# Kernel tuning notes

Measured on AMD Instinct MI355X. Metric: run time of the kernel, lower is better.

## Reference

```python
import jax, jax.numpy as jnp
import numpy as np

N_NODES = 100000
N_EDGES = 1600000
N_GRAPHS = 4096
IN_DIM = 14
HID = 128


def setup_inputs() -> dict:
    key = jax.random.key(0)
    ks = jax.random.split(key, 12)
    x = jax.random.normal(ks[0], (N_NODES, IN_DIM), dtype=jnp.float32)
    edge_index = jax.random.randint(ks[1], (2, N_EDGES), 0, N_NODES, dtype=jnp.int64)
    batch = jnp.sort(jax.random.randint(ks[2], (N_NODES,), 0, N_GRAPHS, dtype=jnp.int64))

    def lin(k, fan_in, fan_out):
        bound = 1.0 / np.sqrt(fan_in)
        kw, kb = jax.random.split(k)
        W = jax.random.uniform(kw, (fan_in, fan_out), minval=-bound, maxval=bound, dtype=jnp.float32)
        b = jax.random.uniform(kb, (fan_out,), minval=-bound, maxval=bound, dtype=jnp.float32)
        return W, b

    W1a, b1a = lin(ks[3], IN_DIM, HID)
    W1b, b1b = lin(ks[4], HID, HID)
    W2a, b2a = lin(ks[5], HID, HID)
    W2b, b2b = lin(ks[6], HID, HID)
    Wout, bout = lin(ks[7], HID, HID)
    return dict(x=x, edge_index=edge_index, batch=batch,
                W1a=W1a, b1a=b1a, W1b=W1b, b1b=b1b,
                W2a=W2a, b2a=b2a, W2b=W2b, b2b=b2b,
                Wout=Wout, bout=bout)


def _gin_conv(x, src, dst, Wa, ba, Wb, bb):
    # aggregate: sum of neighbor features x[src] scattered to dst; eps = 0
    agg = jax.ops.segment_sum(x[src], dst, num_segments=N_NODES)
    h = x + agg  # (1 + eps) * x + sum_j x_j, eps=0
    h = jax.nn.relu(h @ Wa + ba)
    return h @ Wb + bb


def reference(x, edge_index, batch, W1a, b1a, W1b, b1b, W2a, b2a, W2b, b2b, Wout, bout):
    src, dst = edge_index[0], edge_index[1]
    h = jax.nn.relu(_gin_conv(x, src, dst, W1a, b1a, W1b, b1b))
    h = jax.nn.relu(_gin_conv(h, src, dst, W2a, b2a, W2b, b2b))
    # global mean pool over graphs
    sums = jax.ops.segment_sum(h, batch, num_segments=N_GRAPHS)          # [G, HID]
    cnts = jax.ops.segment_sum(jnp.ones((h.shape[0],), h.dtype), batch, num_segments=N_GRAPHS)
    pooled = sums / jnp.maximum(cnts, 1.0)[:, None]
    # dropout is identity in eval mode
    return pooled @ Wout + bout
```

## Files before the change

kernel.cpp:

```cpp
#include <hip/hip_runtime.h>
#include <hip/hip_bf16.h>

#define NODES  100000
#define EDGES  1600000
#define GRAPHS 4096
#define HID    128
#define INDIM  14
#define NPART  8
#define PART_SZ ((NODES + NPART - 1) / NPART)
#define BPG    256
#define CSTRIDE 64
#define LDST   136
#define LDSTF  132

typedef float f32x4 __attribute__((ext_vector_type(4)));
typedef short bf16x8 __attribute__((ext_vector_type(8)));
typedef int   i32x4 __attribute__((ext_vector_type(4)));

__device__ __forceinline__ unsigned packbf(float a, float b) {
    __hip_bfloat162 t;
    t.x = __float2bfloat16(a);
    t.y = __float2bfloat16(b);
    return *(unsigned*)&t;
}
__device__ __forceinline__ void acc8(float* a, uint4 v) {
    a[0] += __uint_as_float(v.x << 16);
    a[1] += __uint_as_float(v.x & 0xffff0000u);
    a[2] += __uint_as_float(v.y << 16);
    a[3] += __uint_as_float(v.y & 0xffff0000u);
    a[4] += __uint_as_float(v.z << 16);
    a[5] += __uint_as_float(v.z & 0xffff0000u);
    a[6] += __uint_as_float(v.w << 16);
    a[7] += __uint_as_float(v.w & 0xffff0000u);
}


__global__ void k_zero2(int* __restrict__ cnt, float* __restrict__ pooled) {
    int i = blockIdx.x * 256 + threadIdx.x;
    if (i < NODES) cnt[i] = 0;
    if (i < GRAPHS * HID) pooled[i] = 0.f;
}


__global__ __launch_bounds__(256) void k_fill_fx(const i32x4* __restrict__ src4,
                                                 const i32x4* __restrict__ dst4,
                                                 int* __restrict__ cnt,
                                                 int* __restrict__ csr) {
    const int g = blockIdx.x & (NPART - 1);
    const int blk = blockIdx.x >> 3;
    const int lo = g * PART_SZ;
    const int n4 = EDGES / 4;
    for (int e4 = blk * 256 + threadIdx.x; e4 < n4; e4 += BPG * 256) {
        i32x4 d = __builtin_nontemporal_load(&dst4[e4]);
        i32x4 s = __builtin_nontemporal_load(&src4[e4]);
#pragma unroll
        for (int j = 0; j < 4; j++) {
            int dj = d[j];
            if ((unsigned)(dj - lo) < PART_SZ) {
                int pos = atomicAdd(&cnt[dj], 1);
                if (pos < CSTRIDE) csr[dj * CSTRIDE + pos] = s[j];
            }
        }
    }
}


__global__ void k_w_cvt4(const float* __restrict__ Wa, const float* __restrict__ Wb,
                         const float* __restrict__ Wc, const float* __restrict__ Wd,
                         __hip_bfloat16* __restrict__ Ta, __hip_bfloat16* __restrict__ Tb,
                         __hip_bfloat16* __restrict__ Tc, __hip_bfloat16* __restrict__ Td) {
    int which = blockIdx.x >> 6;
    int idx = (blockIdx.x & 63) * 256 + threadIdx.x;
    const float* W = which == 0 ? Wa : which == 1 ? Wb : which == 2 ? Wc : Wd;
    __hip_bfloat16* T = which == 0 ? Ta : which == 1 ? Tb : which == 2 ? Tc : Td;
    int n = idx & 127, k = idx >> 7;
    T[n * HID + k] = __float2bfloat16(W[k * HID + n]);
}


template <int RELU, int TO_LDS>
__device__ __forceinline__ void mfma_slice16(const __hip_bfloat16* lds_in,
                                             const __hip_bfloat16* __restrict__ Wt,
                                             const float* __restrict__ bias,
                                             __hip_bfloat16* lds_out,
                                             __hip_bfloat16* __restrict__ gout,
                                             int row0, int tid) {
    const int wave = tid >> 6;
    const int lane = tid & 63;
    const int rl = lane & 15;
    const int kb = lane >> 4;

    bf16x8 afrag[4];
#pragma unroll
    for (int kc = 0; kc < 4; kc++)
        afrag[kc] = *(const bf16x8*)(lds_in + rl * LDST + kc * 32 + kb * 8);

#pragma unroll
    for (int s = 0; s < 2; s++) {
        const int n = wave * 2 + s;
        f32x4 acc = (f32x4){0.f, 0.f, 0.f, 0.f};
        const __hip_bfloat16* Bp = Wt + (size_t)(n * 16 + rl) * HID + kb * 8;
#pragma unroll
        for (int kc = 0; kc < 4; kc++) {
            bf16x8 bfrag = *(const bf16x8*)(Bp + kc * 32);
            acc = __builtin_amdgcn_mfma_f32_16x16x32_bf16(afrag[kc], bfrag, acc, 0, 0, 0);
        }
        const int col = n * 16 + rl;
        const float bv = bias[col];
#pragma unroll
        for (int j = 0; j < 4; j++) {
            int rloc = kb * 4 + j;
            float v = acc[j] + bv;
            if (RELU) v = fmaxf(v, 0.f);
            if (TO_LDS)
                lds_out[rloc * LDST + col] = __float2bfloat16(v);
            else
                gout[(size_t)(row0 + rloc) * HID + col] = __float2bfloat16(v);
        }
    }
}


__global__ __launch_bounds__(256) void k_l1(const float* __restrict__ x,
                                            const int* __restrict__ cnt,
                                            const int* __restrict__ csr,
                                            const float* __restrict__ W1a,
                                            const float* __restrict__ b1a,
                                            const __hip_bfloat16* __restrict__ Wt1b,
                                            const float* __restrict__ b1b,
                                            __hip_bfloat16* __restrict__ h1) {
    __shared__ float p14[16][16];
    __shared__ __hip_bfloat16 t[16 * LDST];
    const int row0 = blockIdx.x * 16;
    const int tid = threadIdx.x;

    {
        int n = tid >> 4, d = tid & 15;
        int node = row0 + n;
        if (d < INDIM) {
            int len = cnt[node];
            if (len > CSTRIDE) len = CSTRIDE;
            const int* cp = csr + (size_t)node * CSTRIDE;
            float acc = x[node * INDIM + d];
            int e = 0;
            for (; e + 7 < len; e += 8) {
                int s0 = cp[e], s1 = cp[e + 1], s2 = cp[e + 2], s3 = cp[e + 3];
                int s4 = cp[e + 4], s5 = cp[e + 5], s6 = cp[e + 6], s7 = cp[e + 7];
                float v0 = x[s0 * INDIM + d], v1 = x[s1 * INDIM + d];
                float v2 = x[s2 * INDIM + d], v3 = x[s3 * INDIM + d];
                float v4 = x[s4 * INDIM + d], v5 = x[s5 * INDIM + d];
                float v6 = x[s6 * INDIM + d], v7 = x[s7 * INDIM + d];
                acc += ((v0 + v1) + (v2 + v3)) + ((v4 + v5) + (v6 + v7));
            }
            for (; e + 3 < len; e += 4) {
                int s0 = cp[e], s1 = cp[e + 1], s2 = cp[e + 2], s3 = cp[e + 3];
                acc += x[s0 * INDIM + d] + x[s1 * INDIM + d] +
                       x[s2 * INDIM + d] + x[s3 * INDIM + d];
            }
            for (; e < len; e++) acc += x[cp[e] * INDIM + d];
            p14[n][d] = acc;
        }
    }
    __syncthreads();

    for (int i = tid; i < 512; i += 256) {
        int r = i >> 5, c4 = (i & 31) << 2;
        float4 bv = *(const float4*)&b1a[c4];
        float ax = bv.x, ay = bv.y, az = bv.z, aw = bv.w;
#pragma unroll
        for (int k = 0; k < INDIM; k++) {
            float a = p14[r][k];
            float4 w = *(const float4*)&W1a[k * HID + c4];
            ax += a * w.x; ay += a * w.y; az += a * w.z; aw += a * w.w;
        }
        unsigned p0 = packbf(fmaxf(ax, 0.f), fmaxf(ay, 0.f));
        unsigned p1 = packbf(fmaxf(az, 0.f), fmaxf(aw, 0.f));
        *(uint2*)&t[r * LDST + c4] = make_uint2(p0, p1);
    }
    __syncthreads();

    mfma_slice16<1, 0>(t, Wt1b, b1b, nullptr, h1, row0, tid);
}


__global__ __launch_bounds__(256) void k_l2p(const uint4* __restrict__ H,
                                             const int* __restrict__ cnt,
                                             const int* __restrict__ csr,
                                             const int* __restrict__ batch,
                                             const __hip_bfloat16* __restrict__ Wt2a,
                                             const float* __restrict__ b2a,
                                             const __hip_bfloat16* __restrict__ Wt2b,
                                             const float* __restrict__ b2b,
                                             float* __restrict__ pooled) {
    __shared__ __hip_bfloat16 ta[16 * LDST];
    __shared__ __hip_bfloat16 tb[16 * LDST];
    __shared__ float t2f[16 * LDSTF];
    __shared__ int sb[16];
    const int row0 = blockIdx.x * 16;
    const int tid = threadIdx.x;

    if (tid < 16) sb[tid] = batch[row0 + tid];

    {
        int n = tid >> 4, q = tid & 15;
        int node = row0 + n;
        int len = cnt[node];
        if (len > CSTRIDE) len = CSTRIDE;
        const int* cp = csr + (size_t)node * CSTRIDE;
        float a[8];
        uint4 v = H[(size_t)node * 16 + q];
        a[0] = __uint_as_float(v.x << 16);
        a[1] = __uint_as_float(v.x & 0xffff0000u);
        a[2] = __uint_as_float(v.y << 16);
        a[3] = __uint_as_float(v.y & 0xffff0000u);
        a[4] = __uint_as_float(v.z << 16);
        a[5] = __uint_as_float(v.z & 0xffff0000u);
        a[6] = __uint_as_float(v.w << 16);
        a[7] = __uint_as_float(v.w & 0xffff0000u);
        int e = 0;
        for (; e + 7 < len; e += 8) {
            uint4 v0 = H[(size_t)cp[e + 0] * 16 + q];
            uint4 v1 = H[(size_t)cp[e + 1] * 16 + q];
            uint4 v2 = H[(size_t)cp[e + 2] * 16 + q];
            uint4 v3 = H[(size_t)cp[e + 3] * 16 + q];
            uint4 v4 = H[(size_t)cp[e + 4] * 16 + q];
            uint4 v5 = H[(size_t)cp[e + 5] * 16 + q];
            uint4 v6 = H[(size_t)cp[e + 6] * 16 + q];
            uint4 v7 = H[(size_t)cp[e + 7] * 16 + q];
            acc8(a, v0); acc8(a, v1); acc8(a, v2); acc8(a, v3);
            acc8(a, v4); acc8(a, v5); acc8(a, v6); acc8(a, v7);
        }
        for (; e + 3 < len; e += 4) {
            uint4 v0 = H[(size_t)cp[e + 0] * 16 + q];
            uint4 v1 = H[(size_t)cp[e + 1] * 16 + q];
            uint4 v2 = H[(size_t)cp[e + 2] * 16 + q];
            uint4 v3 = H[(size_t)cp[e + 3] * 16 + q];
            acc8(a, v0); acc8(a, v1); acc8(a, v2); acc8(a, v3);
        }
        for (; e < len; e++) {
            uint4 vv = H[(size_t)cp[e] * 16 + q];
            acc8(a, vv);
        }
        uint4 o;
        o.x = packbf(a[0], a[1]);
        o.y = packbf(a[2], a[3]);
        o.z = packbf(a[4], a[5]);
        o.w = packbf(a[6], a[7]);
        *(uint4*)&ta[n * LDST + q * 8] = o;
    }
    __syncthreads();

    mfma_slice16<1, 1>(ta, Wt2a, b2a, tb, nullptr, row0, tid);
    __syncthreads();

    {
        const int wave = tid >> 6;
        const int lane = tid & 63;
        const int rl = lane & 15;
        const int kb = lane >> 4;
        bf16x8 afrag[4];
#pragma unroll
        for (int kc = 0; kc < 4; kc++)
            afrag[kc] = *(const bf16x8*)(tb + rl * LDST + kc * 32 + kb * 8);
#pragma unroll
        for (int s = 0; s < 2; s++) {
            const int n = wave * 2 + s;
            f32x4 acc = (f32x4){0.f, 0.f, 0.f, 0.f};
            const __hip_bfloat16* Bp = Wt2b + (size_t)(n * 16 + rl) * HID + kb * 8;
#pragma unroll
            for (int kc = 0; kc < 4; kc++) {
                bf16x8 bfrag = *(const bf16x8*)(Bp + kc * 32);
                acc = __builtin_amdgcn_mfma_f32_16x16x32_bf16(afrag[kc], bfrag, acc, 0, 0, 0);
            }
            const int col = n * 16 + rl;
            const float bv = b2b[col];
#pragma unroll
            for (int j = 0; j < 4; j++)
                t2f[(kb * 4 + j) * LDSTF + col] = fmaxf(acc[j] + bv, 0.f);
        }
    }
    __syncthreads();

    {
        int c = tid & 127;
        int half = tid >> 7;
        int r0 = half * 8;
        float acc = t2f[r0 * LDSTF + c];
        int gprev = sb[r0];
        for (int r = r0 + 1; r < r0 + 8; r++) {
            int g = sb[r];
            float v = t2f[r * LDSTF + c];
            if (g != gprev) {
                atomicAdd(&pooled[(size_t)gprev * HID + c], acc);
                acc = 0.f;
                gprev = g;
            }
            acc += v;
        }
        atomicAdd(&pooled[(size_t)gprev * HID + c], acc);
    }
}


__device__ __forceinline__ int lower_bound_i(const int* __restrict__ a, int n, int key) {
    int lo = 0, hi = n;
    while (lo < hi) {
        int mid = (lo + hi) >> 1;
        if (a[mid] < key) lo = mid + 1; else hi = mid;
    }
    return lo;
}

__global__ __launch_bounds__(256) void k_head(const float* __restrict__ pooled,
                                              const int* __restrict__ batch,
                                              const __hip_bfloat16* __restrict__ Wt,
                                              const float* __restrict__ bias,
                                              float* __restrict__ out) {
    const int wave = threadIdx.x >> 6;
    const int lane = threadIdx.x & 63;
    const int row0 = blockIdx.x * 64 + wave * 16;
    const int rl = lane & 15;
    const int kb = lane >> 4;

    const int g = row0 + rl;
    int lo = lower_bound_i(batch, NODES, g);
    int hi = lower_bound_i(batch, NODES, g + 1);
    float inv = 1.0f / fmaxf((float)(hi - lo), 1.0f);

    bf16x8 afrag[4];
#pragma unroll
    for (int kc = 0; kc < 4; kc++) {
        const float* Ap = pooled + (size_t)g * HID + kc * 32 + kb * 8;
        unsigned u[4];
#pragma unroll
        for (int p = 0; p < 4; p++) u[p] = packbf(Ap[p * 2] * inv, Ap[p * 2 + 1] * inv);
        afrag[kc] = *(bf16x8*)u;
    }

#pragma unroll
    for (int n = 0; n < 8; n++) {
        f32x4 acc = (f32x4){0.f, 0.f, 0.f, 0.f};
        const __hip_bfloat16* Bp = Wt + (size_t)(n * 16 + rl) * HID + kb * 8;
#pragma unroll
        for (int kc = 0; kc < 4; kc++) {
            bf16x8 bfrag = *(const bf16x8*)(Bp + kc * 32);
            acc = __builtin_amdgcn_mfma_f32_16x16x32_bf16(afrag[kc], bfrag, acc, 0, 0, 0);
        }
        const int col = n * 16 + rl;
        const float bv = bias[col];
#pragma unroll
        for (int j = 0; j < 4; j++)
            out[(size_t)(row0 + kb * 4 + j) * HID + col] = acc[j] + bv;
    }
}


extern "C" void kernel_launch(void* const* d_in, const int* in_sizes, int n_in,
                              void* d_out, int out_size, void* d_ws, size_t ws_size,
                              hipStream_t stream) {
    const float* x     = (const float*)d_in[0];
    const int*   ei    = (const int*)d_in[1];
    const int*   batch = (const int*)d_in[2];
    const float* W1a = (const float*)d_in[3];
    const float* b1a = (const float*)d_in[4];
    const float* W1b = (const float*)d_in[5];
    const float* b1b = (const float*)d_in[6];
    const float* W2a = (const float*)d_in[7];
    const float* b2a = (const float*)d_in[8];
    const float* W2b = (const float*)d_in[9];
    const float* b2b = (const float*)d_in[10];
    const float* Wout = (const float*)d_in[11];
    const float* bout = (const float*)d_in[12];

    const int* src = ei;
    const int* dst = ei + EDGES;

    char* w = (char*)d_ws;
    auto alloc = [&](size_t bytes) {
        void* p = (void*)w;
        w += (bytes + 255) & ~(size_t)255;
        return p;
    };
    __hip_bfloat16* h1 = (__hip_bfloat16*)alloc((size_t)NODES * HID * 2);
    int* cnt = (int*)alloc((size_t)NODES * 4);
    float* pooled = (float*)alloc((size_t)GRAPHS * HID * 4);
    __hip_bfloat16* Wt1b = (__hip_bfloat16*)alloc(HID * HID * 2);
    __hip_bfloat16* Wt2a = (__hip_bfloat16*)alloc(HID * HID * 2);
    __hip_bfloat16* Wt2b = (__hip_bfloat16*)alloc(HID * HID * 2);
    __hip_bfloat16* Wtout = (__hip_bfloat16*)alloc(HID * HID * 2);
    int* csr = (int*)alloc((size_t)NODES * CSTRIDE * 4);
    float* out = (float*)d_out;

    k_w_cvt4<<<256, 256, 0, stream>>>(W1b, W2a, W2b, Wout, Wt1b, Wt2a, Wt2b, Wtout);
    k_zero2<<<(GRAPHS * HID + 255) / 256, 256, 0, stream>>>(cnt, pooled);

    k_fill_fx<<<NPART * BPG, 256, 0, stream>>>((const i32x4*)src, (const i32x4*)dst, cnt, csr);

    k_l1<<<NODES / 16, 256, 0, stream>>>(x, cnt, csr, W1a, b1a, Wt1b, b1b, h1);

    k_l2p<<<NODES / 16, 256, 0, stream>>>((const uint4*)h1, cnt, csr, batch,
                                          Wt2a, b2a, Wt2b, b2b, pooled);

    k_head<<<GRAPHS / 64, 256, 0, stream>>>(pooled, batch, Wtout, bout, out);
}
```

Measured before the change: 257.4 us.

## Pad node features to 16 floats for float4 gathers in layer-1 aggregation

The prep kernel now also copies x into a 16-float-padded buffer, so layer 1 can gather neighbor features as four float4 loads per node instead of 14 scalar loads. k_l1 now handles 64 nodes per block with 4 threads per node, and an inline MFMA loop gives each wave 16 rows. This cuts the number of gather instructions and spreads the per-block weight loads over more rows. In exchange it adds an extra padded copy of x and a larger prep launch, and drops the 8-way unrolled gather loop.

Result: slower. 266.9 us (+3.7%).

```diff
diff --git a/kernel.cpp b/kernel.cpp
--- a/kernel.cpp
+++ b/kernel.cpp
@@ -35,10 +35,15 @@
 }
 
 
-__global__ void k_zero2(int* __restrict__ cnt, float* __restrict__ pooled) {
+__global__ void k_prep2(int* __restrict__ cnt, float* __restrict__ pooled,
+                        const float* __restrict__ x, float* __restrict__ xf) {
     int i = blockIdx.x * 256 + threadIdx.x;
     if (i < NODES) cnt[i] = 0;
     if (i < GRAPHS * HID) pooled[i] = 0.f;
+    if (i < NODES * 16) {
+        int node = i >> 4, c = i & 15;
+        xf[i] = c < INDIM ? x[node * INDIM + c] : 0.f;
+    }
 }
 
 
@@ -121,7 +126,7 @@
 }
 
 
-__global__ __launch_bounds__(256) void k_l1(const float* __restrict__ x,
+__global__ __launch_bounds__(256) void k_l1(const float4* __restrict__ xf,
                                             const int* __restrict__ cnt,
                                             const int* __restrict__ csr,
                                             const float* __restrict__ W1a,
@@ -129,41 +134,42 @@
                                             const __hip_bfloat16* __restrict__ Wt1b,
                                             const float* __restrict__ b1b,
                                             __hip_bfloat16* __restrict__ h1) {
-    __shared__ float p14[16][16];
-    __shared__ __hip_bfloat16 t[16 * LDST];
-    const int row0 = blockIdx.x * 16;
+    __shared__ float p14[64][16];
+    __shared__ __hip_bfloat16 t[64 * LDST];
+    const int row0 = blockIdx.x * 64;
     const int tid = threadIdx.x;
 
     {
-        int n = tid >> 4, d = tid & 15;
-        int node = row0 + n;
-        if (d < INDIM) {
+        int nl = tid >> 2, q = tid & 3;
+        int node = row0 + nl;
+        float4 acc = make_float4(0.f, 0.f, 0.f, 0.f);
+        if (node < NODES) {
             int len = cnt[node];
             if (len > CSTRIDE) len = CSTRIDE;
             const int* cp = csr + (size_t)node * CSTRIDE;
-            float acc = x[node * INDIM + d];
+            acc = xf[(size_t)node * 4 + q];
             int e = 0;
-            for (; e + 7 < len; e += 8) {
-                int s0 = cp[e], s1 = cp[e + 1], s2 = cp[e + 2], s3 = cp[e + 3];
-                int s4 = cp[e + 4], s5 = cp[e + 5], s6 = cp[e + 6], s7 = cp[e + 7];
-                float v0 = x[s0 * INDIM + d], v1 = x[s1 * INDIM + d];
-                float v2 = x[s2 * INDIM + d], v3 = x[s3 * INDIM + d];
-                float v4 = x[s4 * INDIM + d], v5 = x[s5 * INDIM + d];
-                float v6 = x[s6 * INDIM + d], v7 = x[s7 * INDIM + d];
-                acc += ((v0 + v1) + (v2 + v3)) + ((v4 + v5) + (v6 + v7));
-            }
             for (; e + 3 < len; e += 4) {
                 int s0 = cp[e], s1 = cp[e + 1], s2 = cp[e + 2], s3 = cp[e + 3];
-                acc += x[s0 * INDIM + d] + x[s1 * INDIM + d] +
-                       x[s2 * INDIM + d] + x[s3 * INDIM + d];
-            }
-            for (; e < len; e++) acc += x[cp[e] * INDIM + d];
-            p14[n][d] = acc;
-        }
+                float4 v0 = xf[(size_t)s0 * 4 + q];
+                float4 v1 = xf[(size_t)s1 * 4 + q];
+                float4 v2 = xf[(size_t)s2 * 4 + q];
+                float4 v3 = xf[(size_t)s3 * 4 + q];
+                acc.x += (v0.x + v1.x) + (v2.x + v3.x);
+                acc.y += (v0.y + v1.y) + (v2.y + v3.y);
+                acc.z += (v0.z + v1.z) + (v2.z + v3.z);
+                acc.w += (v0.w + v1.w) + (v2.w + v3.w);
+            }
+            for (; e < len; e++) {
+                float4 v = xf[(size_t)cp[e] * 4 + q];
+                acc.x += v.x; acc.y += v.y; acc.z += v.z; acc.w += v.w;
+            }
+        }
+        *(float4*)&p14[nl][q * 4] = acc;
     }
     __syncthreads();
 
-    for (int i = tid; i < 512; i += 256) {
+    for (int i = tid; i < 2048; i += 256) {
         int r = i >> 5, c4 = (i & 31) << 2;
         float4 bv = *(const float4*)&b1a[c4];
         float ax = bv.x, ay = bv.y, az = bv.z, aw = bv.w;
@@ -179,7 +185,34 @@
     }
     __syncthreads();
 
-    mfma_slice16<1, 0>(t, Wt1b, b1b, nullptr, h1, row0, tid);
+    {
+        const int wave = tid >> 6;
+        const int lane = tid & 63;
+        const int rl = lane & 15;
+        const int kb = lane >> 4;
+        const __hip_bfloat16* Ap = t + (wave * 16 + rl) * LDST + kb * 8;
+        bf16x8 afrag[4];
+#pragma unroll
+        for (int kc = 0; kc < 4; kc++) afrag[kc] = *(const bf16x8*)(Ap + kc * 32);
+#pragma unroll
+        for (int n = 0; n < 8; n++) {
+            f32x4 acc = (f32x4){0.f, 0.f, 0.f, 0.f};
+            const __hip_bfloat16* Bp = Wt1b + (size_t)(n * 16 + rl) * HID + kb * 8;
+#pragma unroll
+            for (int kc = 0; kc < 4; kc++) {
+                bf16x8 bfrag = *(const bf16x8*)(Bp + kc * 32);
+                acc = __builtin_amdgcn_mfma_f32_16x16x32_bf16(afrag[kc], bfrag, acc, 0, 0, 0);
+            }
+            const int col = n * 16 + rl;
+            const float bv = b1b[col];
+#pragma unroll
+            for (int j = 0; j < 4; j++) {
+                int row = row0 + wave * 16 + kb * 4 + j;
+                if (row < NODES)
+                    h1[(size_t)row * HID + col] = __float2bfloat16(fmaxf(acc[j] + bv, 0.f));
+            }
+        }
+    }
 }
 
 
@@ -382,6 +415,7 @@
         return p;
     };
     __hip_bfloat16* h1 = (__hip_bfloat16*)alloc((size_t)NODES * HID * 2);
+    float* xf = (float*)alloc((size_t)NODES * 16 * 4);
     int* cnt = (int*)alloc((size_t)NODES * 4);
     float* pooled = (float*)alloc((size_t)GRAPHS * HID * 4);
     __hip_bfloat16* Wt1b = (__hip_bfloat16*)alloc(HID * HID * 2);
@@ -392,11 +426,12 @@
     float* out = (float*)d_out;
 
     k_w_cvt4<<<256, 256, 0, stream>>>(W1b, W2a, W2b, Wout, Wt1b, Wt2a, Wt2b, Wtout);
-    k_zero2<<<(GRAPHS * HID + 255) / 256, 256, 0, stream>>>(cnt, pooled);
+    k_prep2<<<(NODES * 16 + 255) / 256, 256, 0, stream>>>(cnt, pooled, x, xf);
 
     k_fill_fx<<<NPART * BPG, 256, 0, stream>>>((const i32x4*)src, (const i32x4*)dst, cnt, csr);
 
-    k_l1<<<NODES / 16, 256, 0, stream>>>(x, cnt, csr, W1a, b1a, Wt1b, b1b, h1);
+    k_l1<<<(NODES + 63) / 64, 256, 0, stream>>>((const float4*)xf, cnt, csr,
+                                                W1a, b1a, Wt1b, b1b, h1);
 
     k_l2p<<<NODES / 16, 256, 0, stream>>>((const uint4*)h1, cnt, csr, batch,
                                           Wt2a, b2a, Wt2b, b2b, pooled);
```
